# Kernel optimization log

Hardware: AMD Instinct MI355X
Metric: run time of the kernel (lower is better)

Reference implementation:

```python
import jax, jax.numpy as jnp
import numpy as np

EMBED_DIM = 512
NUM_HEADS = 8
HEAD_DIM = EMBED_DIM // NUM_HEADS
EDGE_HIDDEN = 512
B, L = 2, 512


def setup_inputs() -> dict:
    key = jax.random.key(0)
    ks = jax.random.split(key, 16)
    s = 0.02
    inp = {
        "query": jax.random.normal(ks[0], (B, L, EMBED_DIM), jnp.float32),
        "key_in": jax.random.normal(ks[1], (B, L, EMBED_DIM), jnp.float32),
        "value": jax.random.normal(ks[2], (B, L, EMBED_DIM), jnp.float32),
        "edge_representation": jax.random.normal(ks[3], (B, L, L), jnp.float32),
        # projection weights stored as [in, out]: y = x @ W + b
        "Wq": jax.random.normal(ks[4], (EMBED_DIM, EMBED_DIM), jnp.float32) * s,
        "bq": jnp.zeros((EMBED_DIM,), jnp.float32),
        "Wk": jax.random.normal(ks[5], (EMBED_DIM, EMBED_DIM), jnp.float32) * s,
        "bk": jnp.zeros((EMBED_DIM,), jnp.float32),
        "Wv": jax.random.normal(ks[6], (EMBED_DIM, EMBED_DIM), jnp.float32) * s,
        "bv": jnp.zeros((EMBED_DIM,), jnp.float32),
        "Wo": jax.random.normal(ks[7], (EMBED_DIM, EMBED_DIM), jnp.float32) * s,
        "bo": jnp.zeros((EMBED_DIM,), jnp.float32),
        # edge MLP: Linear(1 -> 512) -> ReLU -> Linear(512 -> num_heads)
        "We1": jax.random.normal(ks[8], (1, EDGE_HIDDEN), jnp.float32) * s,
        "be1": jnp.zeros((EDGE_HIDDEN,), jnp.float32),
        "We2": jax.random.normal(ks[9], (EDGE_HIDDEN, NUM_HEADS), jnp.float32) * s,
        "be2": jnp.zeros((NUM_HEADS,), jnp.float32),
    }
    return inp


def reference(query, key_in, value, edge_representation,
              Wq, bq, Wk, bk, Wv, bv, Wo, bo, We1, be1, We2, be2):
    Bc, Lc, _ = query.shape
    # project and split heads: [B, H, L, Dh]
    def split_heads(x):
        return x.reshape(Bc, Lc, NUM_HEADS, HEAD_DIM).transpose(0, 2, 1, 3)
    Q = split_heads(query @ Wq + bq)
    K = split_heads(key_in @ Wk + bk)
    V = split_heads(value @ Wv + bv)
    # edge MLP on scalar edge features: [B, L, L, 1] -> [B, L, L, H]
    e = edge_representation[..., None]
    h = jax.nn.relu(e * We1[0] + be1)          # [B, L, L, 512]
    edge_bias = h @ We2 + be2                   # [B, L, L, H]
    scale = 1.0 / jnp.sqrt(jnp.asarray(HEAD_DIM, query.dtype))
    scores = jnp.einsum("bhqd,bhkd->bhqk", Q, K) * scale
    scores = scores + edge_bias.transpose(0, 3, 1, 2)  # [B, H, L, L]
    attn = jax.nn.softmax(scores, axis=-1)
    out = jnp.einsum("bhqk,bhkd->bhqd", attn, V)
    out = out.transpose(0, 2, 1, 3).reshape(Bc, Lc, EMBED_DIM)
    return out @ Wo + bo
```

## Files before the change

### kernel.cpp

```cpp
#include <hip/hip_runtime.h>
#include <hip/hip_bf16.h>

typedef __attribute__((ext_vector_type(8))) short bf16x8;
typedef __attribute__((ext_vector_type(4))) float f32x4;

#define LOG2E 1.44269504088896340736f

#define XQ_OFF 0
#define XK_OFF 524288
#define XV_OFF 1048576
#define WQ_OFF 1572864
#define WK_OFF 1835008
#define WV_OFF 2097152
#define WO_OFF 2359296
#define QB_OFF 2621440
#define KB_OFF 3145728
#define VT_OFF 3670016
#define AO_OFF 4194304
#define T_B   9437184
#define A_B   (T_B + 4096)
#define C_B   (A_B + 20480)
#define SEG_B (C_B + 20480)

__device__ __forceinline__ unsigned short f2bf(float f) {
  union { __hip_bfloat16 h; unsigned short u; } c;
  c.h = __float2bfloat16(f);
  return c.u;
}

__global__ __launch_bounds__(256) void k_convert(
    const float* __restrict__ xq, const float* __restrict__ xk, const float* __restrict__ xv,
    const float* __restrict__ wq, const float* __restrict__ wk, const float* __restrict__ wv,
    const float* __restrict__ wo, unsigned short* __restrict__ wsb) {
  int i = blockIdx.x * 256 + threadIdx.x;
  if (i < 393216) {
    int region = i >> 17;
    int off = i & 131071;
    const float* src = (region == 0) ? xq : (region == 1) ? xk : xv;
    float4 v = ((const float4*)src)[off];
    ushort4 o;
    o.x = f2bf(v.x); o.y = f2bf(v.y); o.z = f2bf(v.z); o.w = f2bf(v.w);
    ((ushort4*)wsb)[i] = o;
  } else {
    int j = i - 393216;
    int region = j >> 16;
    int off = j & 65535;
    const float* src = (region == 0) ? wq : (region == 1) ? wk : (region == 2) ? wv : wo;
    float4 v = ((const float4*)src)[off];
    int flat = off << 2;
    int k = flat >> 9, n = flat & 511;
    unsigned short* dst = wsb + WQ_OFF + region * 262144;
    dst[(n + 0) * 512 + k] = f2bf(v.x);
    dst[(n + 1) * 512 + k] = f2bf(v.y);
    dst[(n + 2) * 512 + k] = f2bf(v.z);
    dst[(n + 3) * 512 + k] = f2bf(v.w);
  }
}

__global__ __launch_bounds__(512) void k_prep(
    const float* __restrict__ w1, const float* __restrict__ b1,
    const float* __restrict__ we2, const float* __restrict__ be2,
    float* __restrict__ wsT, float* __restrict__ wsA, float* __restrict__ wsC) {
  __shared__ float sT[512];
  __shared__ int sIdx[512];
  __shared__ float sDA[512][8];
  __shared__ float sDC[512][8];
  __shared__ float sA0[8], sC0[8];
  int tid = threadIdx.x;
  float w = w1[tid], bb = b1[tid];
  sT[tid] = (w != 0.f) ? (-bb / w) : -3.4e38f;
  sIdx[tid] = tid;
  {
#pragma unroll
    for (int h = 0; h < 8; ++h) {
      float w2 = we2[tid * 8 + h];
      float ra = 0.f, rc = 0.f;
      if (w < 0.f)       { ra = w2 * w; rc = w2 * bb; }
      else if (w == 0.f) { rc = w2 * fmaxf(bb, 0.f); }
      sDA[tid][h] = ra; sDC[tid][h] = rc;
    }
  }
  for (int size = 2; size <= 512; size <<= 1) {
    for (int stride = size >> 1; stride > 0; stride >>= 1) {
      __syncthreads();
      int i = tid, j = tid ^ stride;
      if (j > i) {
        bool up = ((i & size) == 0);
        float ti = sT[i], tj = sT[j];
        if (up ? (ti > tj) : (ti < tj)) {
          sT[i] = tj; sT[j] = ti;
          int t = sIdx[i]; sIdx[i] = sIdx[j]; sIdx[j] = t;
        }
      }
    }
  }
  for (int st = 256; st > 0; st >>= 1) {
    __syncthreads();
    if (tid < st) {
#pragma unroll
      for (int h = 0; h < 8; ++h) { sDA[tid][h] += sDA[tid + st][h]; sDC[tid][h] += sDC[tid + st][h]; }
    }
  }
  __syncthreads();
  if (tid < 8) { sA0[tid] = sDA[0][tid]; sC0[tid] = sDC[0][tid] + be2[tid]; }
  __syncthreads();
  {
    int k = sIdx[tid];
    float wk = w1[k], bk = b1[k];
#pragma unroll
    for (int h = 0; h < 8; ++h) {
      float w2 = we2[k * 8 + h];
      float da = 0.f, dc = 0.f;
      if (wk > 0.f)      { da =  w2 * wk; dc =  w2 * bk; }
      else if (wk < 0.f) { da = -w2 * wk; dc = -w2 * bk; }
      sDA[tid][h] = da; sDC[tid][h] = dc;
    }
  }
  __syncthreads();
  for (int off = 1; off < 512; off <<= 1) {
    float ta[8], tc[8];
    bool act = (tid >= off);
    if (act) {
#pragma unroll
      for (int h = 0; h < 8; ++h) { ta[h] = sDA[tid - off][h]; tc[h] = sDC[tid - off][h]; }
    }
    __syncthreads();
    if (act) {
#pragma unroll
      for (int h = 0; h < 8; ++h) { sDA[tid][h] += ta[h]; sDC[tid][h] += tc[h]; }
    }
    __syncthreads();
  }
  wsT[tid] = sT[tid];
  if (tid < 8) { wsA[tid] = sA0[tid]; wsC[tid] = sC0[tid]; }
#pragma unroll
  for (int h = 0; h < 8; ++h) {
    wsA[(tid + 1) * 8 + h] = sA0[h] + sDA[tid][h];
    wsC[(tid + 1) * 8 + h] = sC0[h] + sDC[tid][h];
  }
}

__global__ __launch_bounds__(256) void k_seg(const float* __restrict__ eg,
                                             const float* __restrict__ wsT,
                                             unsigned short* __restrict__ segp) {
  __shared__ float sT[512];
  int tid = threadIdx.x;
  sT[tid] = wsT[tid];
  sT[tid + 256] = wsT[tid + 256];
  __syncthreads();
  int i = blockIdx.x * 256 + tid;
  float ev = eg[i];
  int lo = 0, hi = 512;
  while (lo < hi) {
    int mid = (lo + hi) >> 1;
    if (sT[mid] < ev) lo = mid + 1; else hi = mid;
  }
  segp[i] = (unsigned short)lo;
}

struct GemmBatch {
  const unsigned short* A;
  const unsigned short* Wt;
  const float* bias;
  void* out;
  int mode;
};

__global__ __launch_bounds__(256) void k_gemm(GemmBatch g0, GemmBatch g1, GemmBatch g2) {
  GemmBatch g = (blockIdx.z == 0) ? g0 : (blockIdx.z == 1) ? g1 : g2;
  const int K = 512;
  int m0 = blockIdx.x * 64, n0 = blockIdx.y * 64;
  int tid = threadIdx.x, wave = tid >> 6, lane = tid & 63;
  int quad = lane >> 4, l16 = lane & 15;
  __shared__ __align__(16) unsigned short sA[64][72];
  __shared__ __align__(16) unsigned short sBt[64][72];
  f32x4 acc[4] = {{0.f,0.f,0.f,0.f},{0.f,0.f,0.f,0.f},{0.f,0.f,0.f,0.f},{0.f,0.f,0.f,0.f}};
  int lr = tid >> 2, ls = tid & 3;
  for (int kb = 0; kb < K; kb += 64) {
    __syncthreads();
    *(uint4*)&sA[lr][ls * 16]      = *(const uint4*)(g.A  + (size_t)(m0 + lr) * K + kb + ls * 16);
    *(uint4*)&sA[lr][ls * 16 + 8]  = *(const uint4*)(g.A  + (size_t)(m0 + lr) * K + kb + ls * 16 + 8);
    *(uint4*)&sBt[lr][ls * 16]     = *(const uint4*)(g.Wt + (size_t)(n0 + lr) * K + kb + ls * 16);
    *(uint4*)&sBt[lr][ls * 16 + 8] = *(const uint4*)(g.Wt + (size_t)(n0 + lr) * K + kb + ls * 16 + 8);
    __syncthreads();
    for (int ks = 0; ks < 2; ++ks) {
      bf16x8 af = *(const bf16x8*)&sA[wave * 16 + l16][ks * 32 + quad * 8];
      for (int nt = 0; nt < 4; ++nt) {
        bf16x8 bf = *(const bf16x8*)&sBt[nt * 16 + l16][ks * 32 + quad * 8];
        acc[nt] = __builtin_amdgcn_mfma_f32_16x16x32_bf16(af, bf, acc[nt], 0, 0, 0);
      }
    }
  }
  int mbase = m0 + wave * 16 + quad * 4;
  for (int nt = 0; nt < 4; ++nt) {
    int n = n0 + nt * 16 + l16;
    float bv = g.bias[n];
    for (int r = 0; r < 4; ++r) {
      float v = acc[nt][r] + bv;
      int m = mbase + r;
      if (g.mode == 0) {
        int b = m >> 9, l = m & 511, hh = n >> 6, d = n & 63;
        ((unsigned short*)g.out)[(((size_t)(b * 8 + hh) * 512) + l) * 64 + d] = f2bf(v);
      } else if (g.mode == 1) {
        ((float*)g.out)[(size_t)m * 512 + n] = v;
      } else {
        int b = m >> 9, l = m & 511, hh = n >> 6, d = n & 63;
        ((unsigned short*)g.out)[(((size_t)(b * 8 + hh) * 64) + d) * 512 + l] = f2bf(v);
      }
    }
  }
}

__global__ __launch_bounds__(256) void k_attn(
    const unsigned short* __restrict__ Qb, const unsigned short* __restrict__ Kb,
    const unsigned short* __restrict__ Vt, const float* __restrict__ eg,
    const unsigned short* __restrict__ segp,
    const float* __restrict__ wsA, const float* __restrict__ wsC,
    unsigned short* __restrict__ ao) {
  int qt = blockIdx.x, h = blockIdx.y, b = blockIdx.z;
  int bh = b * 8 + h;
  int q0 = qt * 16;
  int tid = threadIdx.x, wave = tid >> 6, lane = tid & 63;
  int quad = lane >> 4, l16 = lane & 15;
  __shared__ float sAh[513], sCh[513];
  __shared__ __align__(16) unsigned short sP[4][16][36];
  __shared__ float sO[4][4][16][16];
  __shared__ float sM[4][16], sL[4][16];
  for (int i = tid; i < 513; i += 256) { sAh[i] = wsA[i * 8 + h]; sCh[i] = wsC[i * 8 + h]; }
  const unsigned short* qp = Qb + ((size_t)bh * 512 + q0 + l16) * 64 + quad * 8;
  bf16x8 qf0 = *(const bf16x8*)qp;
  bf16x8 qf1 = *(const bf16x8*)(qp + 32);
  int key_base = wave * 128;
  f32x4 S[4][2];
#pragma unroll
  for (int kt = 0; kt < 4; ++kt) {
    int key0 = key_base + kt * 32;
#pragma unroll
    for (int half = 0; half < 2; ++half) {
      const unsigned short* kp = Kb + ((size_t)bh * 512 + key0 + half * 16 + l16) * 64 + quad * 8;
      bf16x8 kf0 = *(const bf16x8*)kp;
      bf16x8 kf1 = *(const bf16x8*)(kp + 32);
      f32x4 acc = {0.f, 0.f, 0.f, 0.f};
      acc = __builtin_amdgcn_mfma_f32_16x16x32_bf16(qf0, kf0, acc, 0, 0, 0);
      acc = __builtin_amdgcn_mfma_f32_16x16x32_bf16(qf1, kf1, acc, 0, 0, 0);
      S[kt][half] = acc;
    }
  }
  __syncthreads();
#pragma unroll
  for (int kt = 0; kt < 4; ++kt)
#pragma unroll
    for (int half = 0; half < 2; ++half)
#pragma unroll
      for (int r = 0; r < 4; ++r) {
        int eidx = (b * 512 + q0 + quad * 4 + r) * 512 + key_base + kt * 32 + half * 16 + l16;
        float ev = eg[eidx];
        int sg = segp[eidx];
        S[kt][half][r] = S[kt][half][r] * 0.125f + sAh[sg] * ev + sCh[sg];
      }
  float m_w[4], l_w[4];
#pragma unroll
  for (int r = 0; r < 4; ++r) {
    float mx = -3.4e38f;
#pragma unroll
    for (int kt = 0; kt < 4; ++kt) { mx = fmaxf(mx, fmaxf(S[kt][0][r], S[kt][1][r])); }
    for (int off = 1; off < 16; off <<= 1) mx = fmaxf(mx, __shfl_xor(mx, off, 64));
    float s = 0.f;
#pragma unroll
    for (int kt = 0; kt < 4; ++kt)
#pragma unroll
      for (int half = 0; half < 2; ++half) {
        float p = exp2f((S[kt][half][r] - mx) * LOG2E);
        S[kt][half][r] = p; s += p;
      }
    for (int off = 1; off < 16; off <<= 1) s += __shfl_xor(s, off, 64);
    m_w[r] = mx; l_w[r] = s;
  }
  f32x4 Oacc[4] = {{0.f,0.f,0.f,0.f},{0.f,0.f,0.f,0.f},{0.f,0.f,0.f,0.f},{0.f,0.f,0.f,0.f}};
#pragma unroll
  for (int kt = 0; kt < 4; ++kt) {
    int key0 = key_base + kt * 32;
#pragma unroll
    for (int half = 0; half < 2; ++half)
#pragma unroll
      for (int r = 0; r < 4; ++r)
        sP[wave][quad * 4 + r][half * 16 + l16] = f2bf(S[kt][half][r]);
    __builtin_amdgcn_wave_barrier();
    bf16x8 pf = *(const bf16x8*)&sP[wave][l16][quad * 8];
    __builtin_amdgcn_wave_barrier();
#pragma unroll
    for (int nt = 0; nt < 4; ++nt) {
      bf16x8 vf = *(const bf16x8*)(Vt + ((size_t)bh * 64 + nt * 16 + l16) * 512 + key0 + quad * 8);
      Oacc[nt] = __builtin_amdgcn_mfma_f32_16x16x32_bf16(pf, vf, Oacc[nt], 0, 0, 0);
    }
  }
  if (l16 == 0) {
#pragma unroll
    for (int r = 0; r < 4; ++r) { sM[wave][quad * 4 + r] = m_w[r]; sL[wave][quad * 4 + r] = l_w[r]; }
  }
#pragma unroll
  for (int nt = 0; nt < 4; ++nt)
#pragma unroll
    for (int r = 0; r < 4; ++r)
      sO[wave][nt][quad * 4 + r][l16] = Oacc[nt][r];
  __syncthreads();
#pragma unroll
  for (int r = 0; r < 4; ++r) {
    int row = quad * 4 + r;
    float M = fmaxf(fmaxf(sM[0][row], sM[1][row]), fmaxf(sM[2][row], sM[3][row]));
    float L = 0.f, Ov = 0.f;
#pragma unroll
    for (int wv = 0; wv < 4; ++wv) {
      float f = exp2f((sM[wv][row] - M) * LOG2E);
      L += f * sL[wv][row];
      Ov += f * sO[wv][wave][row][l16];
    }
    float v = Ov / L;
    ao[((size_t)(b * 512 + q0 + row)) * 512 + h * 64 + wave * 16 + l16] = f2bf(v);
  }
}

extern "C" void kernel_launch(void* const* d_in, const int* in_sizes, int n_in,
                              void* d_out, int out_size, void* d_ws, size_t ws_size,
                              hipStream_t stream) {
  const float* q   = (const float*)d_in[0];
  const float* kin = (const float*)d_in[1];
  const float* v   = (const float*)d_in[2];
  const float* eg  = (const float*)d_in[3];
  const float* Wq  = (const float*)d_in[4];
  const float* bq  = (const float*)d_in[5];
  const float* Wk  = (const float*)d_in[6];
  const float* bk  = (const float*)d_in[7];
  const float* Wv  = (const float*)d_in[8];
  const float* bv  = (const float*)d_in[9];
  const float* Wo  = (const float*)d_in[10];
  const float* bo  = (const float*)d_in[11];
  const float* We1 = (const float*)d_in[12];
  const float* be1 = (const float*)d_in[13];
  const float* We2 = (const float*)d_in[14];
  const float* be2 = (const float*)d_in[15];
  unsigned short* wsb = (unsigned short*)d_ws;
  float* wsT = (float*)((char*)d_ws + T_B);
  float* wsA = (float*)((char*)d_ws + A_B);
  float* wsC = (float*)((char*)d_ws + C_B);
  unsigned short* segp = (unsigned short*)((char*)d_ws + SEG_B);

  k_convert<<<2560, 256, 0, stream>>>(q, kin, v, Wq, Wk, Wv, Wo, wsb);
  k_prep<<<1, 512, 0, stream>>>(We1, be1, We2, be2, wsT, wsA, wsC);
  k_seg<<<2048, 256, 0, stream>>>(eg, wsT, segp);
  GemmBatch gq{wsb + XQ_OFF, wsb + WQ_OFF, bq, (void*)(wsb + QB_OFF), 0};
  GemmBatch gk{wsb + XK_OFF, wsb + WK_OFF, bk, (void*)(wsb + KB_OFF), 0};
  GemmBatch gv{wsb + XV_OFF, wsb + WV_OFF, bv, (void*)(wsb + VT_OFF), 2};
  k_gemm<<<dim3(16, 8, 3), 256, 0, stream>>>(gq, gk, gv);
  k_attn<<<dim3(32, 8, 2), 256, 0, stream>>>(wsb + QB_OFF, wsb + KB_OFF, wsb + VT_OFF,
                                             eg, segp, wsA, wsC, wsb + AO_OFF);
  GemmBatch go{wsb + AO_OFF, wsb + WO_OFF, bo, d_out, 1};
  k_gemm<<<dim3(16, 8, 1), 256, 0, stream>>>(go, go, go);
}
```

Before: 149.9 us.

## Fuse conversion and segment kernels, transpose weights through shared-memory tiles

Merges the bf16 conversion kernel and the edge-segment binary-search kernel into one launch, so a kernel launch and its inter-kernel gap disappear. The weight transpose now goes through 64x64 shared-memory tiles with 16-byte coalesced stores instead of scattered 2-byte global writes. The risk is a heterogeneous grid whose block types differ in cost, plus the work now depends on k_prep finishing first.

New measurement: 141.6 us. 1.06x faster.

```diff
diff --git a/kernel.cpp b/kernel.cpp
--- a/kernel.cpp
+++ b/kernel.cpp
@@ -28,35 +28,6 @@
   return c.u;
 }
 
-__global__ __launch_bounds__(256) void k_convert(
-    const float* __restrict__ xq, const float* __restrict__ xk, const float* __restrict__ xv,
-    const float* __restrict__ wq, const float* __restrict__ wk, const float* __restrict__ wv,
-    const float* __restrict__ wo, unsigned short* __restrict__ wsb) {
-  int i = blockIdx.x * 256 + threadIdx.x;
-  if (i < 393216) {
-    int region = i >> 17;
-    int off = i & 131071;
-    const float* src = (region == 0) ? xq : (region == 1) ? xk : xv;
-    float4 v = ((const float4*)src)[off];
-    ushort4 o;
-    o.x = f2bf(v.x); o.y = f2bf(v.y); o.z = f2bf(v.z); o.w = f2bf(v.w);
-    ((ushort4*)wsb)[i] = o;
-  } else {
-    int j = i - 393216;
-    int region = j >> 16;
-    int off = j & 65535;
-    const float* src = (region == 0) ? wq : (region == 1) ? wk : (region == 2) ? wv : wo;
-    float4 v = ((const float4*)src)[off];
-    int flat = off << 2;
-    int k = flat >> 9, n = flat & 511;
-    unsigned short* dst = wsb + WQ_OFF + region * 262144;
-    dst[(n + 0) * 512 + k] = f2bf(v.x);
-    dst[(n + 1) * 512 + k] = f2bf(v.y);
-    dst[(n + 2) * 512 + k] = f2bf(v.z);
-    dst[(n + 3) * 512 + k] = f2bf(v.w);
-  }
-}
-
 __global__ __launch_bounds__(512) void k_prep(
     const float* __restrict__ w1, const float* __restrict__ b1,
     const float* __restrict__ we2, const float* __restrict__ be2,
@@ -140,22 +111,58 @@
   }
 }
 
-__global__ __launch_bounds__(256) void k_seg(const float* __restrict__ eg,
-                                             const float* __restrict__ wsT,
-                                             unsigned short* __restrict__ segp) {
-  __shared__ float sT[512];
-  int tid = threadIdx.x;
-  sT[tid] = wsT[tid];
-  sT[tid + 256] = wsT[tid + 256];
-  __syncthreads();
-  int i = blockIdx.x * 256 + tid;
-  float ev = eg[i];
-  int lo = 0, hi = 512;
-  while (lo < hi) {
-    int mid = (lo + hi) >> 1;
-    if (sT[mid] < ev) lo = mid + 1; else hi = mid;
-  }
-  segp[i] = (unsigned short)lo;
+__global__ __launch_bounds__(256) void k_pre(
+    const float* __restrict__ xq, const float* __restrict__ xk, const float* __restrict__ xv,
+    const float* __restrict__ wq, const float* __restrict__ wk, const float* __restrict__ wv,
+    const float* __restrict__ wo, const float* __restrict__ eg,
+    const float* __restrict__ wsT, unsigned short* __restrict__ wsb,
+    unsigned short* __restrict__ segp) {
+  __shared__ __align__(16) char smem[64 * 68 * 2];
+  int blk = blockIdx.x, tid = threadIdx.x;
+  if (blk < 256) {
+    unsigned short (*sWt)[68] = (unsigned short (*)[68])smem;
+    int mat = blk >> 6, tile = blk & 63;
+    int k0 = (tile >> 3) * 64, n0 = (tile & 7) * 64;
+    const float* src = (mat == 0) ? wq : (mat == 1) ? wk : (mat == 2) ? wv : wo;
+    int row = tid >> 2, cq = tid & 3;
+    const float4* sp = (const float4*)(src + (size_t)(k0 + row) * 512 + n0 + cq * 16);
+#pragma unroll
+    for (int j = 0; j < 4; ++j) {
+      float4 v = sp[j];
+      int nl = cq * 16 + j * 4;
+      sWt[nl + 0][row] = f2bf(v.x);
+      sWt[nl + 1][row] = f2bf(v.y);
+      sWt[nl + 2][row] = f2bf(v.z);
+      sWt[nl + 3][row] = f2bf(v.w);
+    }
+    __syncthreads();
+    int n = tid >> 2, kq = tid & 3;
+    unsigned short* dst = wsb + WQ_OFF + mat * 262144 + (size_t)(n0 + n) * 512 + k0 + kq * 16;
+    *(uint4*)dst       = *(const uint4*)&sWt[n][kq * 16];
+    *(uint4*)(dst + 8) = *(const uint4*)&sWt[n][kq * 16 + 8];
+  } else if (blk < 1792) {
+    int i = (blk - 256) * 256 + tid;
+    int region = i >> 17;
+    int off = i & 131071;
+    const float* src = (region == 0) ? xq : (region == 1) ? xk : xv;
+    float4 v = ((const float4*)src)[off];
+    ushort4 o;
+    o.x = f2bf(v.x); o.y = f2bf(v.y); o.z = f2bf(v.z); o.w = f2bf(v.w);
+    ((ushort4*)wsb)[i] = o;
+  } else {
+    float* sT = (float*)smem;
+    sT[tid] = wsT[tid];
+    sT[tid + 256] = wsT[tid + 256];
+    __syncthreads();
+    int i = (blk - 1792) * 256 + tid;
+    float ev = eg[i];
+    int lo = 0, hi = 512;
+    while (lo < hi) {
+      int mid = (lo + hi) >> 1;
+      if (sT[mid] < ev) lo = mid + 1; else hi = mid;
+    }
+    segp[i] = (unsigned short)lo;
+  }
 }
 
 struct GemmBatch {
@@ -345,9 +352,8 @@
   float* wsC = (float*)((char*)d_ws + C_B);
   unsigned short* segp = (unsigned short*)((char*)d_ws + SEG_B);
 
-  k_convert<<<2560, 256, 0, stream>>>(q, kin, v, Wq, Wk, Wv, Wo, wsb);
   k_prep<<<1, 512, 0, stream>>>(We1, be1, We2, be2, wsT, wsA, wsC);
-  k_seg<<<2048, 256, 0, stream>>>(eg, wsT, segp);
+  k_pre<<<3840, 256, 0, stream>>>(q, kin, v, Wq, Wk, Wv, Wo, eg, wsT, wsb, segp);
   GemmBatch gq{wsb + XQ_OFF, wsb + WQ_OFF, bq, (void*)(wsb + QB_OFF), 0};
   GemmBatch gk{wsb + XK_OFF, wsb + WK_OFF, bk, (void*)(wsb + KB_OFF), 0};
   GemmBatch gv{wsb + XV_OFF, wsb + WV_OFF, bv, (void*)(wsb + VT_OFF), 2};
```
